# Kernel tuning notes

Hardware: AMD Instinct MI355X
Metric: run time of the kernel (lower is better)

The kernel has to match this reference:

```python
import jax, jax.numpy as jnp
import numpy as np

B, C, ANGRES, H, W = 4, 60, 5, 96, 96
N = ANGRES * ANGRES  # 25 angular views
D = C                # dims = channels in TrippleAttention


def _norm(x, axis):
    # torch F.normalize: x / max(||x||_2, 1e-12)
    n = jnp.linalg.norm(x, axis=axis, keepdims=True)
    return x / jnp.maximum(n, 1e-12)


def setup_inputs() -> dict:
    key = jax.random.key(0)
    ks = jax.random.split(key, 8)
    s = 0.02
    return {
        "x": jax.random.normal(ks[0], (B, C, N, H, W), jnp.float32),
        "w_spa_q": jax.random.normal(ks[1], (D, C), jnp.float32) * s,      # 1x1 conv, stride 1
        "w_spa_kv": jax.random.normal(ks[2], (2 * D, C), jnp.float32) * s, # 1x1 conv, stride 2
        "w_ang_qkv": jax.random.normal(ks[3], (3 * D, C), jnp.float32) * s,
        "w_fre_qkv": jax.random.normal(ks[4], (3 * D, C), jnp.float32) * s,
        "ln_gamma": jnp.ones((3 * D,), jnp.float32),
        "ln_beta": jnp.zeros((3 * D,), jnp.float32),
        "w_mlp1": jax.random.normal(ks[5], (C, 3 * D), jnp.float32) * s,   # torch Linear [out,in]
        "w_mlp2": jax.random.normal(ks[6], (C, C), jnp.float32) * s,
    }


def reference(x, w_spa_q, w_spa_kv, w_ang_qkv, w_fre_qkv, ln_gamma, ln_beta, w_mlp1, w_mlp2):
    b, c, n, h, w = x.shape
    d = w_spa_q.shape[0]

    # ---- SpatialAttention ----
    # q: stride-1 1x1 conv then '(b n) c h w -> b (h w) (c n)'
    sq = jnp.einsum('dc,bcnhw->bhwdn', w_spa_q, x).reshape(b, h * w, d * n)
    xs = x[:, :, :, ::2, ::2]                       # stride-2, kernel-1 conv == subsample
    h2, w2 = xs.shape[3], xs.shape[4]
    skv = jnp.einsum('dc,bcnhw->bdnhw', w_spa_kv, xs)
    sk = skv[:, :d].reshape(b, d * n, h2 * w2)       # 'b (c n) (h w)'
    sv = skv[:, d:].transpose(0, 3, 4, 1, 2).reshape(b, h2 * w2, d * n)  # 'b (h w) (c n)'
    sq = _norm(sq, -1)
    sk = _norm(sk, -2)
    s_att = jax.nn.softmax(sq @ sk, axis=-1)         # [b, hw, h2w2]
    s_fea = (s_att @ sv).reshape(b, h, w, d, n).transpose(0, 3, 4, 1, 2)  # [b,d,n,h,w]

    # ---- AngularAttention ----
    aqkv = jnp.einsum('dc,bcnhw->bdnhw', w_ang_qkv, x)
    aq = aqkv[:, :d].transpose(0, 2, 1, 3, 4).reshape(b, n, d * h * w)       # 'b (u v) (c h w)'
    ak = aqkv[:, d:2 * d].transpose(0, 1, 3, 4, 2).reshape(b, d * h * w, n)  # 'b (c h w) (u v)'
    av = aqkv[:, 2 * d:].transpose(0, 2, 1, 3, 4).reshape(b, n, d * h * w)
    aq = _norm(aq, -1)
    ak = _norm(ak, -2)
    a_att = jax.nn.softmax(aq @ ak, axis=-1)         # [b, n, n]
    a_fea = (a_att @ av).reshape(b, n, d, h, w).transpose(0, 2, 1, 3, 4)     # [b,d,n,h,w]

    # ---- FrequencyAttention (use_mask=False) ----
    fqkv = jnp.einsum('dc,bcnhw->bdnhw', w_fre_qkv, x)
    fq = fqkv[:, :d].reshape(b, d, n * h * w)        # 'b c (n h w)'
    fk = fqkv[:, d:2 * d].reshape(b, d, n * h * w).transpose(0, 2, 1)        # 'b (n h w) c'
    fv = fqkv[:, 2 * d:].reshape(b, d, n * h * w)
    fq = _norm(fq, -1)
    fk = _norm(fk, -2)
    f_att = jax.nn.softmax(fq @ fk, axis=-1)         # [b, d, d]
    f_fea = (f_att @ fv).reshape(b, d, n, h, w)

    # ---- concat + MLP (dropout is identity at inference) ----
    cat = jnp.concatenate([s_fea, a_fea, f_fea], axis=1)  # [b, 3d, n, h, w]
    t = cat.transpose(0, 3, 4, 2, 1)                      # [b, h, w, n, 3d]
    mu = t.mean(-1, keepdims=True)
    var = t.var(-1, keepdims=True)                        # biased var, matching torch LayerNorm
    t = (t - mu) / jnp.sqrt(var + 1e-5) * ln_gamma + ln_beta
    t = jax.nn.relu(t @ w_mlp1.T)
    t = t @ w_mlp2.T                                      # [b, h, w, n, c]
    return t.transpose(0, 4, 3, 1, 2) + x
```

## Files before the change

kernel.cpp:

```cpp
#include <hip/hip_runtime.h>
#include <hip/hip_bf16.h>

typedef unsigned short u16;
typedef float f32x4 __attribute__((ext_vector_type(4)));
typedef short s16x8 __attribute__((ext_vector_type(8)));


__device__ __forceinline__ float b2f(u16 u) {
  union { unsigned int i; float f; } v; v.i = ((unsigned int)u) << 16; return v.f;
}
__device__ __forceinline__ u16 f2b(float f) {
  union { float f; unsigned int i; } v; v.f = f;
  unsigned int i = v.i + 0x7FFFu + ((v.i >> 16) & 1u);
  return (u16)(i >> 16);
}

__global__ void fallback_copy(const float* __restrict__ x, float* __restrict__ out, size_t n) {
  size_t i = (size_t)blockIdx.x * 256 + threadIdx.x;
  size_t st = (size_t)gridDim.x * 256;
  for (; i < n; i += st) out[i] = x[i];
}

__global__ __launch_bounds__(256) void cast_x(const float* __restrict__ xb, u16* __restrict__ Xb) {
  size_t e = ((size_t)blockIdx.x * 256 + threadIdx.x) * 4;
  ushort4 o;
  if (e < 13824000) {
    float4 v = *(const float4*)(xb + e);
    o.x = f2b(v.x); o.y = f2b(v.y); o.z = f2b(v.z); o.w = f2b(v.w);
  } else { o.x = 0; o.y = 0; o.z = 0; o.w = 0; }
  *(ushort4*)(Xb + e) = o;
}

__global__ __launch_bounds__(256) void proj_full(const float* __restrict__ xb,
    const float* __restrict__ Wq, const float* __restrict__ Wang,
    const float* __restrict__ Wfre, u16* __restrict__ PF) {
  int s = blockIdx.x * 256 + threadIdx.x;
  int grp = blockIdx.y;
  const float* W = (grp == 0) ? Wq : ((grp == 1) ? (Wang + 7200) : (Wfre + 7200));
  const float* xs = xb + s;
  float xr[60];
#pragma unroll
  for (int c = 0; c < 60; ++c) xr[c] = xs[(size_t)c * 230400];
  u16* ob = PF + (size_t)grp * 13824000 + s;
  for (int r0 = 0; r0 < 60; r0 += 4) {
    const float* w0 = W + r0 * 60;
    const float* w1 = w0 + 60;
    const float* w2 = w0 + 120;
    const float* w3 = w0 + 180;
    float a0 = 0.f, a1 = 0.f, a2 = 0.f, a3 = 0.f;
#pragma unroll
    for (int c = 0; c < 60; ++c) {
      float xv = xr[c];
      a0 += w0[c] * xv; a1 += w1[c] * xv; a2 += w2[c] * xv; a3 += w3[c] * xv;
    }
    ob[(size_t)(r0    ) * 230400] = f2b(a0);
    ob[(size_t)(r0 + 1) * 230400] = f2b(a1);
    ob[(size_t)(r0 + 2) * 230400] = f2b(a2);
    ob[(size_t)(r0 + 3) * 230400] = f2b(a3);
  }
}

__global__ __launch_bounds__(256) void proj_sub(const float* __restrict__ xb,
    const float* __restrict__ Wkv, u16* __restrict__ PS) {
  int s2 = blockIdx.x * 256 + threadIdx.x;
  int grp = blockIdx.y;
  int nn = s2 / 2304; int rem = s2 - nn * 2304;
  int hy = rem / 48;  int hx = rem - hy * 48;
  const float* xs = xb + (size_t)nn * 9216 + hy * 192 + hx * 2;
  float xr[60];
#pragma unroll
  for (int c = 0; c < 60; ++c) xr[c] = xs[(size_t)c * 230400];
  u16* ob = PS + (size_t)grp * 1728000 + s2;
  const float* Wg = Wkv + grp * 1800;
  for (int r0 = 0; r0 < 30; r0 += 5) {
    const float* w0 = Wg + r0 * 60;
    const float* w1 = w0 + 60;
    const float* w2 = w0 + 120;
    const float* w3 = w0 + 180;
    const float* w4 = w0 + 240;
    float a0 = 0.f, a1 = 0.f, a2 = 0.f, a3 = 0.f, a4 = 0.f;
#pragma unroll
    for (int c = 0; c < 60; ++c) {
      float xv = xr[c];
      a0 += w0[c] * xv; a1 += w1[c] * xv; a2 += w2[c] * xv;
      a3 += w3[c] * xv; a4 += w4[c] * xv;
    }
    ob[(size_t)(r0    ) * 57600] = f2b(a0);
    ob[(size_t)(r0 + 1) * 57600] = f2b(a1);
    ob[(size_t)(r0 + 2) * 57600] = f2b(a2);
    ob[(size_t)(r0 + 3) * 57600] = f2b(a3);
    ob[(size_t)(r0 + 4) * 57600] = f2b(a4);
  }
}

__global__ __launch_bounds__(256) void norm_sums(const u16* __restrict__ inb,
    float* __restrict__ partials, int S) {
  int s = blockIdx.x * 256 + threadIdx.x;
  int fc = blockIdx.y;
  const u16* p = inb + (size_t)(fc * 60) * S + s;
  float a0 = 0.f, a1 = 0.f, a2 = 0.f, a3 = 0.f;
#pragma unroll
  for (int f = 0; f < 60; f += 4) {
    float v0 = b2f(p[(size_t)(f + 0) * S]); a0 += v0 * v0;
    float v1 = b2f(p[(size_t)(f + 1) * S]); a1 += v1 * v1;
    float v2 = b2f(p[(size_t)(f + 2) * S]); a2 += v2 * v2;
    float v3 = b2f(p[(size_t)(f + 3) * S]); a3 += v3 * v3;
  }
  partials[(size_t)fc * S + s] = (a0 + a1) + (a2 + a3);
}

__global__ __launch_bounds__(256) void transpose_scale(const u16* __restrict__ inb,
    const float* __restrict__ partials, u16* __restrict__ outb, int S) {
  __shared__ float Ts[64 * 65];
  __shared__ float rinv[64];
  int s0 = blockIdx.x * 64, f0 = blockIdx.y * 64;
  int t = threadIdx.x; int sl = t & 63; int g = t >> 6;
  if (t < 64) {
    float tot = 0.f;
    for (int c = 0; c < 25; ++c) tot += partials[(size_t)c * S + s0 + t];
    rinv[t] = 1.f / fmaxf(sqrtf(tot), 1e-12f);
  }
  for (int e = t; e < 4096; e += 256) {
    int fr = e >> 6, sc = e & 63; int f = f0 + fr;
    Ts[fr * 65 + sc] = (f < 1500) ? b2f(inb[(size_t)f * S + s0 + sc]) : 0.f;
  }
  __syncthreads();
  for (int sr = g; sr < 64; sr += 4) {
    float v = Ts[sl * 65 + sr] * rinv[sr];
    outb[(size_t)(s0 + sr) * 1536 + f0 + sl] = f2b(v);
  }
}

template<int M, int N, int K, int EPI>
__global__ __launch_bounds__(256) void gemm_bt(const u16* __restrict__ A,
    const u16* __restrict__ BT, void* __restrict__ C) {
  __shared__ __align__(16) u16 As[128 * 40];
  __shared__ __align__(16) u16 Bs[128 * 40];
  const int tid = threadIdx.x;
  const int bm = blockIdx.x, bn = blockIdx.y;
  const int lane = tid & 63;
  const int wv = tid >> 6;
  const int wm = (wv >> 1) * 64, wn = (wv & 1) * 64;
  const int lm = lane & 15, lq = lane >> 4;
  f32x4 z = {0.f, 0.f, 0.f, 0.f};
  f32x4 acc[4][4];
#pragma unroll
  for (int i = 0; i < 4; ++i)
#pragma unroll
    for (int j = 0; j < 4; ++j) acc[i][j] = z;

  for (int k0 = 0; k0 < K; k0 += 32) {
    __syncthreads();
#pragma unroll
    for (int r = 0; r < 4; ++r) {
      int idx = tid + (r << 8);
      int row = (idx >> 2) & 127;
      int seg = idx & 3;
      if (r < 2) {
        const uint4* src = (const uint4*)(A + (size_t)(bm * 128 + row) * K + k0 + seg * 8);
        *(uint4*)&As[row * 40 + seg * 8] = *src;
      } else {
        const uint4* src = (const uint4*)(BT + (size_t)(bn * 128 + row) * K + k0 + seg * 8);
        *(uint4*)&Bs[row * 40 + seg * 8] = *src;
      }
    }
    __syncthreads();
    s16x8 af[4], bf[4];
#pragma unroll
    for (int i = 0; i < 4; ++i)
      af[i] = *(const s16x8*)&As[(wm + i * 16 + lm) * 40 + lq * 8];
#pragma unroll
    for (int j = 0; j < 4; ++j)
      bf[j] = *(const s16x8*)&Bs[(wn + j * 16 + lm) * 40 + lq * 8];
#pragma unroll
    for (int i = 0; i < 4; ++i)
#pragma unroll
      for (int j = 0; j < 4; ++j)
        acc[i][j] = __builtin_amdgcn_mfma_f32_16x16x32_bf16(af[i], bf[j], acc[i][j], 0, 0, 0);
  }

#pragma unroll
  for (int i = 0; i < 4; ++i) {
    int row0 = bm * 128 + wm + i * 16 + lq * 4;
#pragma unroll
    for (int j = 0; j < 4; ++j) {
      int col = bn * 128 + wn + j * 16 + lm;
      if (EPI == 0) {
        float* Cb = (float*)C;
#pragma unroll
        for (int r = 0; r < 4; ++r)
          Cb[(size_t)(row0 + r) * N + col] = acc[i][j][r];
      } else {
        if (col < 1500) {
          u16* Cb = (u16*)C;
          uint2 pk;
          pk.x = (unsigned int)f2b(acc[i][j][0]) | ((unsigned int)f2b(acc[i][j][1]) << 16);
          pk.y = (unsigned int)f2b(acc[i][j][2]) | ((unsigned int)f2b(acc[i][j][3]) << 16);
          *(uint2*)&Cb[(size_t)col * M + row0] = pk;
        }
      }
    }
  }
}

__global__ __launch_bounds__(256) void softmax_rows(const float* __restrict__ L,
                                                    u16* __restrict__ att) {
  size_t row = blockIdx.x;
  const float* Lr = L + row * 2304;
  u16* ar = att + row * 2304;
  int t = threadIdx.x;
  float v[9]; float mx = -1e30f;
#pragma unroll
  for (int i = 0; i < 9; ++i) { v[i] = Lr[t + i * 256]; mx = fmaxf(mx, v[i]); }
  __shared__ float red[256];
  red[t] = mx; __syncthreads();
  for (int st = 128; st > 0; st >>= 1) { if (t < st) red[t] = fmaxf(red[t], red[t + st]); __syncthreads(); }
  mx = red[0]; __syncthreads();
  float s = 0.f;
#pragma unroll
  for (int i = 0; i < 9; ++i) { v[i] = __expf(v[i] - mx); s += v[i]; }
  red[t] = s; __syncthreads();
  for (int st = 128; st > 0; st >>= 1) { if (t < st) red[t] += red[t + st]; __syncthreads(); }
  float rs = 1.f / red[0];
#pragma unroll
  for (int i = 0; i < 9; ++i) ar[t + i * 256] = f2b(v[i] * rs);
}

__global__ __launch_bounds__(256) void ang_dots(const float* __restrict__ G,
    const float* __restrict__ Ma_g, const float* __restrict__ Mq_g,
    const float* __restrict__ Mk_g, float* __restrict__ dots) {
  int p = blockIdx.x;
  const float* m; int ri, ci;
  if (p < 625)      { m = Ma_g; ri = p / 25; ci = p % 25; }
  else if (p < 650) { m = Mq_g; ri = p - 625; ci = ri; }
  else              { m = Mk_g; ri = p - 650; ci = ri; }
  int t = threadIdx.x;
  float a = 0.f;
  for (int e = t; e < 3600; e += 256) {
    int c = e / 60, cp = e - c * 60;
    a += m[e] * G[(size_t)(c * 25 + ri) * 1536 + cp * 25 + ci];
  }
  __shared__ float red[256];
  red[t] = a; __syncthreads();
  for (int st = 128; st > 0; st >>= 1) { if (t < st) red[t] += red[t + st]; __syncthreads(); }
  if (t == 0) dots[p] = red[0];
}

__global__ __launch_bounds__(64) void ang_finish(const float* __restrict__ dots,
                                                 float* __restrict__ Aatt) {
  int t = threadIdx.x;
  if (t < 25) {
    float rq = 1.f / fmaxf(sqrtf(dots[625 + t]), 1e-12f);
    float l[25], mx = -1e30f;
    for (int j = 0; j < 25; ++j) {
      float rk = 1.f / fmaxf(sqrtf(dots[650 + j]), 1e-12f);
      l[j] = dots[t * 25 + j] * rq * rk;
      mx = fmaxf(mx, l[j]);
    }
    float s = 0.f;
    for (int j = 0; j < 25; ++j) { l[j] = __expf(l[j] - mx); s += l[j]; }
    float rs = 1.f / s;
    for (int j = 0; j < 25; ++j) Aatt[t * 25 + j] = l[j] * rs;
  }
}

__global__ __launch_bounds__(256) void fre_gs(const float* __restrict__ G,
                                              float* __restrict__ Gs) {
  int e = blockIdx.x * 256 + threadIdx.x;
  if (e >= 3600) return;
  int c = e / 60, cp = e - c * 60;
  const float* base = G + (size_t)(c * 25) * 1536 + cp * 25;
  float a = 0.f;
#pragma unroll
  for (int n = 0; n < 25; ++n) a += base[(size_t)n * 1537];
  Gs[e] = a;
}

__global__ __launch_bounds__(256) void fre_finish(const float* __restrict__ Gs_g,
    const float* __restrict__ Wfre, float* __restrict__ Fatt) {
  __shared__ float Gs[3600], T1q[3600], T1k[3600];
  __shared__ float qn[60], kn[60];
  int t = threadIdx.x;
  for (int e = t; e < 3600; e += 256) Gs[e] = Gs_g[e];
  __syncthreads();
  for (int e = t; e < 3600; e += 256) {
    int u = e / 60, cp = e % 60;
    const float* wq = Wfre + u * 60;
    const float* wk = Wfre + 3600 + u * 60;
    float aq = 0.f, ak = 0.f;
    for (int c = 0; c < 60; ++c) { float g = Gs[c * 60 + cp]; aq += wq[c] * g; ak += wk[c] * g; }
    T1q[e] = aq; T1k[e] = ak;
  }
  __syncthreads();
  for (int e = t; e < 3600; e += 256) {
    int u = e / 60, v = e % 60;
    const float* wk = Wfre + 3600 + v * 60;
    float a = 0.f;
    for (int cp = 0; cp < 60; ++cp) a += T1q[u * 60 + cp] * wk[cp];
    Gs[e] = a;
  }
  for (int u = t; u < 60; u += 256) {
    const float* wq = Wfre + u * 60;
    const float* wk = Wfre + 3600 + u * 60;
    float aq = 0.f, ak = 0.f;
    for (int cp = 0; cp < 60; ++cp) { aq += T1q[u * 60 + cp] * wq[cp]; ak += T1k[u * 60 + cp] * wk[cp]; }
    qn[u] = aq; kn[u] = ak;
  }
  __syncthreads();
  if (t < 60) {
    float rq = 1.f / fmaxf(sqrtf(qn[t]), 1e-12f);
    float l[60], mx = -1e30f;
    for (int v = 0; v < 60; ++v) {
      float rk = 1.f / fmaxf(sqrtf(kn[v]), 1e-12f);
      l[v] = Gs[t * 60 + v] * rq * rk;
      mx = fmaxf(mx, l[v]);
    }
    float s = 0.f;
    for (int v = 0; v < 60; ++v) { l[v] = __expf(l[v] - mx); s += l[v]; }
    float rs = 1.f / s;
    for (int v = 0; v < 60; ++v) Fatt[t * 60 + v] = l[v] * rs;
  }
}

__global__ __launch_bounds__(256) void a_fea(const u16* __restrict__ PF,
    const float* __restrict__ Aatt, u16* __restrict__ CAT) {
  int hw = blockIdx.x * 256 + threadIdx.x;
  int dd = blockIdx.y;
  const u16* V = PF + ((size_t)(60 + dd)) * 230400 + hw;
  float v[25];
#pragma unroll
  for (int j = 0; j < 25; ++j) v[j] = b2f(V[(size_t)j * 9216]);
  u16* ob = CAT + (size_t)(1500 + dd * 25) * 9216 + hw;
  for (int i = 0; i < 25; ++i) {
    float a = 0.f;
#pragma unroll
    for (int j = 0; j < 25; ++j) a += Aatt[i * 25 + j] * v[j];
    ob[(size_t)i * 9216] = f2b(a);
  }
}

__global__ __launch_bounds__(256) void f_fea(const u16* __restrict__ PF,
    const float* __restrict__ Fatt, u16* __restrict__ CAT) {
  int s = blockIdx.x * 256 + threadIdx.x;
  const u16* V = PF + (size_t)120 * 230400 + s;
  float v[60];
#pragma unroll
  for (int u = 0; u < 60; ++u) v[u] = b2f(V[(size_t)u * 230400]);
  u16* ob = CAT + (size_t)27648000 + s;
  for (int u = 0; u < 60; ++u) {
    float a = 0.f;
#pragma unroll
    for (int vv = 0; vv < 60; ++vv) a += Fatt[u * 60 + vv] * v[vv];
    ob[(size_t)u * 230400] = f2b(a);
  }
}

__global__ void precompute(const float* __restrict__ W1, const float* __restrict__ W2,
    const float* __restrict__ gamma, const float* __restrict__ beta,
    const float* __restrict__ Wang,
    float* __restrict__ Avec, float* __restrict__ Btvec,
    float* __restrict__ W1T, float* __restrict__ W2T,
    float* __restrict__ Ma, float* __restrict__ Mq, float* __restrict__ Mk) {
  int t = threadIdx.x;
  for (int e = t; e < 10800; e += 256) { int q = e / 60, j = e % 60; W1T[e] = W1[j * 180 + q]; }
  for (int e = t; e < 3600;  e += 256) { int j = e / 60, k = e % 60; W2T[e] = W2[k * 60 + j]; }
  for (int e = t; e < 3600; e += 256) {
    int c = e / 60, cp = e % 60;
    const float* Waq = Wang;
    const float* Wak = Wang + 3600;
    float ma = 0.f, mq = 0.f, mk = 0.f;
    for (int d = 0; d < 60; ++d) {
      float q = Waq[d * 60 + c], qp = Waq[d * 60 + cp];
      float k = Wak[d * 60 + c], kp = Wak[d * 60 + cp];
      ma += q * kp; mq += q * qp; mk += k * kp;
    }
    Ma[e] = ma; Mq[e] = mq; Mk[e] = mk;
  }
  if (t < 60) {
    float a = 0.f, bt = 0.f;
    for (int q = 0; q < 180; ++q) { a += gamma[q] * W1[t * 180 + q]; bt += beta[q] * W1[t * 180 + q]; }
    Avec[t] = a; Btvec[t] = bt;
  }
}

__global__ __launch_bounds__(256) void fuse_ln_mlp(const u16* __restrict__ CAT,
    const float* __restrict__ xb, const float* __restrict__ gamma,
    const float* __restrict__ W1T, const float* __restrict__ W2T,
    const float* __restrict__ Avec, const float* __restrict__ Btvec,
    float* __restrict__ outb) {
  int s = blockIdx.x * 256 + threadIdx.x;
  const u16* cb = CAT + s;
  float S1[60];
#pragma unroll
  for (int j = 0; j < 60; ++j) S1[j] = 0.f;
  float sum = 0.f, sq = 0.f;
  for (int q = 0; q < 180; ++q) {
    float val = b2f(cb[(size_t)q * 230400]);
    sum += val; sq += val * val;
    float u = val * gamma[q];
    const float* w = W1T + q * 60;
#pragma unroll
    for (int j = 0; j < 60; ++j) S1[j] += u * w[j];
  }
  float mu = sum * (1.f / 180.f);
  float var = sq * (1.f / 180.f) - mu * mu;
  float inv = rsqrtf(var + 1e-5f);
  float y2[60];
#pragma unroll
  for (int k = 0; k < 60; ++k) y2[k] = 0.f;
  for (int j = 0; j < 60; ++j) {
    float y1 = inv * (S1[j] - mu * Avec[j]) + Btvec[j];
    y1 = fmaxf(y1, 0.f);
    const float* w = W2T + j * 60;
#pragma unroll
    for (int k = 0; k < 60; ++k) y2[k] += y1 * w[k];
  }
  const float* xs = xb + s;
  float* ob = outb + s;
#pragma unroll
  for (int k = 0; k < 60; ++k) ob[(size_t)k * 230400] = y2[k] + xs[(size_t)k * 230400];
}

extern "C" void kernel_launch(void* const* d_in, const int* in_sizes, int n_in,
                              void* d_out, int out_size, void* d_ws, size_t ws_size,
                              hipStream_t stream) {
  const float* x        = (const float*)d_in[0];
  const float* w_spa_q  = (const float*)d_in[1];
  const float* w_spa_kv = (const float*)d_in[2];
  const float* w_ang    = (const float*)d_in[3];
  const float* w_fre    = (const float*)d_in[4];
  const float* ln_gamma = (const float*)d_in[5];
  const float* ln_beta  = (const float*)d_in[6];
  const float* w_mlp1   = (const float*)d_in[7];
  const float* w_mlp2   = (const float*)d_in[8];
  float* out = (float*)d_out;
  (void)in_sizes; (void)n_in; (void)out_size;

  char* ws = (char*)d_ws;
  const size_t A1 = 0;
  const size_t A1_PS = 82944256;
  const size_t A2 = 96934656;
  const size_t A3 = 139401984;
  size_t off = 224336640;
  auto alloc = [&](size_t bytes) -> void* {
    void* p = ws + off; off = (off + bytes + 255) & ~(size_t)255; return p;
  };
  float* Aatt  = (float*)alloc(4 * 625 * 4);
  float* Fatt  = (float*)alloc(4 * 3600 * 4);
  float* Adots = (float*)alloc(4 * 675 * 4);
  float* Gsg   = (float*)alloc(4 * 3600 * 4);
  float* Avec  = (float*)alloc(240);
  float* Btvec = (float*)alloc(240);
  float* W1T   = (float*)alloc(43200);
  float* W2T   = (float*)alloc(14400);
  float* Ma    = (float*)alloc(14400);
  float* Mq    = (float*)alloc(14400);
  float* Mk    = (float*)alloc(14400);

  if (off > ws_size) {
    fallback_copy<<<4096, 256, 0, stream>>>(x, out, (size_t)55296000);
    return;
  }

  u16*   PF  = (u16*)(ws + A1);
  u16*   PS  = (u16*)(ws + A1_PS);
  float* G2  = (float*)(ws + A2);
  u16*   sqn = (u16*)(ws + A2);
  u16*   skn = (u16*)(ws + A2 + 28311552);
  u16*   att = (u16*)(ws + A2);
  u16*   Xb  = (u16*)(ws + A3);
  float* L   = (float*)(ws + A3);
  u16*   CAT = (u16*)(ws + A3);
  float* Pbig   = (float*)(ws + A3);
  float* Psmall = (float*)(ws + A3 + 921600);

  precompute<<<1, 256, 0, stream>>>(w_mlp1, w_mlp2, ln_gamma, ln_beta, w_ang,
                                    Avec, Btvec, W1T, W2T, Ma, Mq, Mk);

  for (int b = 0; b < 4; ++b) {
    const float* xb = x + (size_t)b * 13824000;
    float* outb = out + (size_t)b * 13824000;

    cast_x<<<13824, 256, 0, stream>>>(xb, Xb);
    gemm_bt<1536, 1536, 9216, 0><<<dim3(12, 12), 256, 0, stream>>>(Xb, Xb, G2);
    ang_dots<<<675, 256, 0, stream>>>(G2, Ma, Mq, Mk, Adots + b * 675);
    ang_finish<<<1, 64, 0, stream>>>(Adots + b * 675, Aatt + b * 625);
    fre_gs<<<15, 256, 0, stream>>>(G2, Gsg + b * 3600);
    fre_finish<<<1, 256, 0, stream>>>(Gsg + b * 3600, w_fre, Fatt + b * 3600);

    proj_full<<<dim3(900, 3), 256, 0, stream>>>(xb, w_spa_q, w_ang, w_fre, PF);
    proj_sub<<<dim3(225, 4), 256, 0, stream>>>(xb, w_spa_kv, PS);

    norm_sums<<<dim3(36, 25), 256, 0, stream>>>(PF, Pbig, 9216);
    transpose_scale<<<dim3(144, 24), 256, 0, stream>>>(PF, Pbig, sqn, 9216);
    norm_sums<<<dim3(9, 25), 256, 0, stream>>>(PS, Psmall, 2304);
    transpose_scale<<<dim3(36, 24), 256, 0, stream>>>(PS, Psmall, skn, 2304);

    gemm_bt<9216, 2304, 1536, 0><<<dim3(72, 18), 256, 0, stream>>>(sqn, skn, L);
    softmax_rows<<<9216, 256, 0, stream>>>(L, att);
    gemm_bt<9216, 1536, 2304, 2><<<dim3(72, 12), 256, 0, stream>>>(att, PS + 3456000, CAT);

    a_fea<<<dim3(36, 60), 256, 0, stream>>>(PF, Aatt + b * 625, CAT);
    f_fea<<<900, 256, 0, stream>>>(PF, Fatt + b * 3600, CAT);

    fuse_ln_mlp<<<900, 256, 0, stream>>>(CAT, xb, ln_gamma, W1T, W2T, Avec, Btvec, outb);
  }
}
```

Before: 4.226 ms.

## Batch Gram GEMM across all batches with split-K and hoist from per-batch loop

```diff
diff --git a/kernel.cpp b/kernel.cpp
--- a/kernel.cpp
+++ b/kernel.cpp
@@ -29,6 +29,81 @@
     o.x = f2b(v.x); o.y = f2b(v.y); o.z = f2b(v.z); o.w = f2b(v.w);
   } else { o.x = 0; o.y = 0; o.z = 0; o.w = 0; }
   *(ushort4*)(Xb + e) = o;
+}
+
+__global__ __launch_bounds__(256) void gram_gemm(const u16* __restrict__ Xall,
+                                                 float* __restrict__ Pg) {
+  __shared__ __align__(16) u16 As[128 * 40];
+  __shared__ __align__(16) u16 Bs[128 * 40];
+  const int z = blockIdx.z;
+  const int b = z >> 1, kk = z & 1;
+  const u16* A = Xall + (size_t)b * 14155776;
+  float* C = Pg + (size_t)z * 2359296;
+  const int tid = threadIdx.x;
+  const int bm = blockIdx.x, bn = blockIdx.y;
+  const int lane = tid & 63;
+  const int wv = tid >> 6;
+  const int wm = (wv >> 1) * 64, wn = (wv & 1) * 64;
+  const int lm = lane & 15, lq = lane >> 4;
+  f32x4 z4 = {0.f, 0.f, 0.f, 0.f};
+  f32x4 acc[4][4];
+#pragma unroll
+  for (int i = 0; i < 4; ++i)
+#pragma unroll
+    for (int j = 0; j < 4; ++j) acc[i][j] = z4;
+
+  const int kbeg = kk * 4608, kend = kbeg + 4608;
+  for (int k0 = kbeg; k0 < kend; k0 += 32) {
+    __syncthreads();
+#pragma unroll
+    for (int r = 0; r < 4; ++r) {
+      int idx = tid + (r << 8);
+      int row = (idx >> 2) & 127;
+      int seg = idx & 3;
+      if (r < 2) {
+        const uint4* src = (const uint4*)(A + (size_t)(bm * 128 + row) * 9216 + k0 + seg * 8);
+        *(uint4*)&As[row * 40 + seg * 8] = *src;
+      } else {
+        const uint4* src = (const uint4*)(A + (size_t)(bn * 128 + row) * 9216 + k0 + seg * 8);
+        *(uint4*)&Bs[row * 40 + seg * 8] = *src;
+      }
+    }
+    __syncthreads();
+    s16x8 af[4], bf[4];
+#pragma unroll
+    for (int i = 0; i < 4; ++i)
+      af[i] = *(const s16x8*)&As[(wm + i * 16 + lm) * 40 + lq * 8];
+#pragma unroll
+    for (int j = 0; j < 4; ++j)
+      bf[j] = *(const s16x8*)&Bs[(wn + j * 16 + lm) * 40 + lq * 8];
+#pragma unroll
+    for (int i = 0; i < 4; ++i)
+#pragma unroll
+      for (int j = 0; j < 4; ++j)
+        acc[i][j] = __builtin_amdgcn_mfma_f32_16x16x32_bf16(af[i], bf[j], acc[i][j], 0, 0, 0);
+  }
+
+#pragma unroll
+  for (int i = 0; i < 4; ++i) {
+    int row0 = bm * 128 + wm + i * 16 + lq * 4;
+#pragma unroll
+    for (int j = 0; j < 4; ++j) {
+      int col = bn * 128 + wn + j * 16 + lm;
+#pragma unroll
+      for (int r = 0; r < 4; ++r)
+        C[(size_t)(row0 + r) * 1536 + col] = acc[i][j][r];
+    }
+  }
+}
+
+__global__ __launch_bounds__(256) void reduce_g2(const float* __restrict__ Pg,
+                                                 float* __restrict__ G2all) {
+  int b = blockIdx.y;
+  size_t r = ((size_t)blockIdx.x * 256 + threadIdx.x) * 4;
+  float4 a = *(const float4*)(Pg + (size_t)(2 * b) * 2359296 + r);
+  float4 c = *(const float4*)(Pg + (size_t)(2 * b + 1) * 2359296 + r);
+  float4 o; o.x = a.x + c.x; o.y = a.y + c.y; o.z = a.z + c.z; o.w = a.w + c.w;
+  *(float4*)(G2all + (size_t)b * 2359296 + r) = o;
 }
 
 __global__ __launch_bounds__(256) void proj_full(const float* __restrict__ xb,
@@ -226,10 +301,13 @@
   for (int i = 0; i < 9; ++i) ar[t + i * 256] = f2b(v[i] * rs);
 }
 
-__global__ __launch_bounds__(256) void ang_dots(const float* __restrict__ G,
+__global__ __launch_bounds__(256) void ang_dots(const float* __restrict__ G2all,
     const float* __restrict__ Ma_g, const float* __restrict__ Mq_g,
-    const float* __restrict__ Mk_g, float* __restrict__ dots) {
+    const float* __restrict__ Mk_g, float* __restrict__ dotsAll) {
   int p = blockIdx.x;
+  int b = blockIdx.y;
+  const float* G = G2all + (size_t)b * 2359296;
+  float* dots = dotsAll + b * 675;
   const float* m; int ri, ci;
   if (p < 625)      { m = Ma_g; ri = p / 25; ci = p % 25; }
   else if (p < 650) { m = Mq_g; ri = p - 625; ci = ri; }
@@ -246,8 +324,11 @@
   if (t == 0) dots[p] = red[0];
 }
 
-__global__ __launch_bounds__(64) void ang_finish(const float* __restrict__ dots,
-                                                 float* __restrict__ Aatt) {
+__global__ __launch_bounds__(64) void ang_finish(const float* __restrict__ dotsAll,
+                                                 float* __restrict__ AattAll) {
+  int b = blockIdx.x;
+  const float* dots = dotsAll + b * 675;
+  float* Aatt = AattAll + b * 625;
   int t = threadIdx.x;
   if (t < 25) {
     float rq = 1.f / fmaxf(sqrtf(dots[625 + t]), 1e-12f);
@@ -264,22 +345,27 @@
   }
 }
 
-__global__ __launch_bounds__(256) void fre_gs(const float* __restrict__ G,
-                                              float* __restrict__ Gs) {
+__global__ __launch_bounds__(256) void fre_gs(const float* __restrict__ G2all,
+                                              float* __restrict__ GsAll) {
   int e = blockIdx.x * 256 + threadIdx.x;
+  int b = blockIdx.y;
   if (e >= 3600) return;
+  const float* G = G2all + (size_t)b * 2359296;
   int c = e / 60, cp = e - c * 60;
   const float* base = G + (size_t)(c * 25) * 1536 + cp * 25;
   float a = 0.f;
 #pragma unroll
   for (int n = 0; n < 25; ++n) a += base[(size_t)n * 1537];
-  Gs[e] = a;
-}
-
-__global__ __launch_bounds__(256) void fre_finish(const float* __restrict__ Gs_g,
-    const float* __restrict__ Wfre, float* __restrict__ Fatt) {
+  GsAll[b * 3600 + e] = a;
+}
+
+__global__ __launch_bounds__(256) void fre_finish(const float* __restrict__ GsAll,
+    const float* __restrict__ Wfre, float* __restrict__ FattAll) {
   __shared__ float Gs[3600], T1q[3600], T1k[3600];
   __shared__ float qn[60], kn[60];
+  int b = blockIdx.x;
+  const float* Gs_g = GsAll + b * 3600;
+  float* Fatt = FattAll + b * 3600;
   int t = threadIdx.x;
   for (int e = t; e < 3600; e += 256) Gs[e] = Gs_g[e];
   __syncthreads();
@@ -462,13 +548,15 @@
     return;
   }
 
+  u16*   XbAll = (u16*)(ws);
+  float* Pg    = (float*)(ws + 113246208);
+  float* G2all = (float*)(ws);
+
   u16*   PF  = (u16*)(ws + A1);
   u16*   PS  = (u16*)(ws + A1_PS);
-  float* G2  = (float*)(ws + A2);
   u16*   sqn = (u16*)(ws + A2);
   u16*   skn = (u16*)(ws + A2 + 28311552);
   u16*   att = (u16*)(ws + A2);
-  u16*   Xb  = (u16*)(ws + A3);
   float* L   = (float*)(ws + A3);
   u16*   CAT = (u16*)(ws + A3);
   float* Pbig   = (float*)(ws + A3);
@@ -477,16 +565,18 @@
   precompute<<<1, 256, 0, stream>>>(w_mlp1, w_mlp2, ln_gamma, ln_beta, w_ang,
                                     Avec, Btvec, W1T, W2T, Ma, Mq, Mk);
 
+  for (int b = 0; b < 4; ++b)
+    cast_x<<<13824, 256, 0, stream>>>(x + (size_t)b * 13824000, XbAll + (size_t)b * 14155776);
+  gram_gemm<<<dim3(12, 12, 8), 256, 0, stream>>>(XbAll, Pg);
+  reduce_g2<<<dim3(2304, 4), 256, 0, stream>>>(Pg, G2all);
+  ang_dots<<<dim3(675, 4), 256, 0, stream>>>(G2all, Ma, Mq, Mk, Adots);
+  ang_finish<<<4, 64, 0, stream>>>(Adots, Aatt);
+  fre_gs<<<dim3(15, 4), 256, 0, stream>>>(G2all, Gsg);
+  fre_finish<<<4, 256, 0, stream>>>(Gsg, w_fre, Fatt);
+
   for (int b = 0; b < 4; ++b) {
     const float* xb = x + (size_t)b * 13824000;
     float* outb = out + (size_t)b * 13824000;
-
-    cast_x<<<13824, 256, 0, stream>>>(xb, Xb);
-    gemm_bt<1536, 1536, 9216, 0><<<dim3(12, 12), 256, 0, stream>>>(Xb, Xb, G2);
-    ang_dots<<<675, 256, 0, stream>>>(G2, Ma, Mq, Mk, Adots + b * 675);
-    ang_finish<<<1, 64, 0, stream>>>(Adots + b * 675, Aatt + b * 625);
-    fre_gs<<<15, 256, 0, stream>>>(G2, Gsg + b * 3600);
-    fre_finish<<<1, 256, 0, stream>>>(Gsg + b * 3600, w_fre, Fatt + b * 3600);
 
     proj_full<<<dim3(900, 3), 256, 0, stream>>>(xb, w_spa_q, w_ang, w_fre, PF);
     proj_sub<<<dim3(225, 4), 256, 0, stream>>>(xb, w_spa_kv, PS);
```

Result: faster. 3.725 ms (-11.9%).
